# Kernel tuning notes

Measured on AMD Instinct MI355X. Metric: run time of the kernel, lower is better.

The kernel has to match this reference:

```python
import jax, jax.numpy as jnp
import numpy as np

K = 4
EPS = 1e-5
NEG_SLOPE = 0.2


def _edge_feature(coor_q, x_q, coor_k, x_k, k):
    """coor_*: [B,3,G*], x_q: [B,C,Gq], x_k: [B,C,Gk] -> [B,2C,Gq,k]"""
    B = x_k.shape[0]
    cq = jax.lax.stop_gradient(coor_q)
    ck = jax.lax.stop_gradient(coor_k)
    # squared pairwise distances [B, Gq, Gk]
    q2 = jnp.sum(cq * cq, axis=1)  # [B,Gq]
    k2 = jnp.sum(ck * ck, axis=1)  # [B,Gk]
    dist = q2[:, :, None] + k2[:, None, :] - 2.0 * jnp.einsum('bcq,bck->bqk', cq, ck)
    _, idx = jax.lax.top_k(-dist, k)  # k nearest, idx: [B,Gq,k]
    xk_t = jnp.transpose(x_k, (0, 2, 1))  # [B,Gk,C]
    feat = xk_t[jnp.arange(B)[:, None, None], idx]  # [B,Gq,k,C] gather
    feat = jnp.transpose(feat, (0, 3, 1, 2))  # [B,C,Gq,k]
    xq = jnp.broadcast_to(x_q[:, :, :, None], feat.shape)
    return jnp.concatenate([feat - xq, xq], axis=1)


def _group_norm(x, gamma, beta, groups):
    # x: [B,C,G,k], normalize per (group, sample) over (C//groups, G, k)
    B, C, G, k = x.shape
    xr = x.reshape(B, groups, -1)
    mean = jnp.mean(xr, axis=-1, keepdims=True)
    var = jnp.var(xr, axis=-1, keepdims=True)
    xn = ((xr - mean) * jax.lax.rsqrt(var + EPS)).reshape(B, C, G, k)
    return xn * gamma[None, :, None, None] + beta[None, :, None, None]


def _block(x, W, gamma, beta):
    # 1x1 conv (no bias) + GroupNorm(4) + LeakyReLU(0.2)
    y = jnp.einsum('oc,bcgk->bogk', W, x)
    y = _group_norm(y, gamma, beta, 4)
    return jax.nn.leaky_relu(y, NEG_SLOPE)


def setup_inputs() -> dict:
    key = jax.random.key(0)
    ks = jax.random.split(key, 10)
    B, C, Gs, Gd = 16, 384, 4096, 1024
    return {
        'coor': jax.random.normal(ks[0], (B, 3, Gs), jnp.float32),
        'f': jax.random.normal(ks[1], (B, C, Gs), jnp.float32),
        'coor_q': jax.random.normal(ks[2], (B, 3, Gd), jnp.float32),
        'f_q': jax.random.normal(ks[3], (B, C, Gd), jnp.float32),
        'W1': jax.random.normal(ks[4], (512, 2 * C), jnp.float32) * 0.02,
        'g1': jnp.ones((512,), jnp.float32),
        'b1': jnp.zeros((512,), jnp.float32),
        'W2': jax.random.normal(ks[5], (C, 1024), jnp.float32) * 0.02,
        'g2': jnp.ones((C,), jnp.float32),
        'b2': jnp.zeros((C,), jnp.float32),
    }


def reference(coor, f, coor_q, f_q, W1, g1, b1, W2, g2, b2):
    e1 = _edge_feature(coor_q, f_q, coor, f, K)        # [B,768,Gd,k]
    h = jnp.max(_block(e1, W1, g1, b1), axis=-1)       # [B,512,Gd]
    e2 = _edge_feature(coor_q, h, coor_q, h, K)        # [B,1024,Gd,k]
    out = jnp.max(_block(e2, W2, g2, b2), axis=-1)     # [B,384,Gd]
    return out
```

## Files before the change

kernel.cpp:

```cpp
#include <hip/hip_runtime.h>
#include <stdint.h>

#define B_   16
#define CIN  384
#define GS   4096
#define GD   1024
#define M1   512
#define K2C  512
#define M2   384
#define NEG  0.2f
#define EPS_ 1e-5f

typedef __bf16 bf16x8 __attribute__((ext_vector_type(8)));
typedef float  f32x4  __attribute__((ext_vector_type(4)));

__device__ __forceinline__ float bf2f(ushort u) {
  uint32_t v = ((uint32_t)u) << 16;
  return __builtin_bit_cast(float, v);
}
__device__ __forceinline__ ushort f2bf(float f) {
  uint32_t x = __builtin_bit_cast(uint32_t, f);
  x += 0x7FFFu + ((x >> 16) & 1u);
  return (ushort)(x >> 16);
}

__global__ void k_transpose(const float* __restrict__ src, ushort* __restrict__ dst,
                            int Cdim, int N) {
  __shared__ ushort tile[32][33];
  int b = blockIdx.z;
  int n0 = blockIdx.x * 32, c0 = blockIdx.y * 32;
  const float* s = src + (size_t)b * Cdim * N;
  ushort* d = dst + (size_t)b * Cdim * N;
  int tx = threadIdx.x, ty = threadIdx.y;
#pragma unroll
  for (int i = 0; i < 4; i++) {
    int c = c0 + ty + i * 8;
    tile[ty + i * 8][tx] = f2bf(s[(size_t)c * N + n0 + tx]);
  }
  __syncthreads();
#pragma unroll
  for (int i = 0; i < 4; i++) {
    int n = n0 + ty + i * 8;
    d[(size_t)n * Cdim + c0 + tx] = tile[tx][ty + i * 8];
  }
}

__global__ void k_wprep(const float* __restrict__ W, ushort* __restrict__ Wa,
                        ushort* __restrict__ Wd, int Khalf) {
  int t = blockIdx.x * 256 + threadIdx.x;
  int o = t / Khalf, c = t % Khalf;
  float wa = W[(size_t)o * 2 * Khalf + c];
  float wb = W[(size_t)o * 2 * Khalf + Khalf + c];
  Wa[t] = f2bf(wa);
  Wd[t] = f2bf(wb - wa);
}

__device__ __forceinline__ void knn_lmin(float& ad, int& ai, float bd, int bi) {
  bool bl = (bd < ad) || (bd == ad && bi < ai);
  ad = bl ? bd : ad; ai = bl ? bi : ai;
}
__device__ __forceinline__ void knn_ce(float& ad, int& ai, float& bd, int& bi) {
  bool bl = (bd < ad) || (bd == ad && bi < ai);
  float na = bl ? bd : ad, nb = bl ? ad : bd;
  int nia = bl ? bi : ai, nib = bl ? ai : bi;
  ad = na; bd = nb; ai = nia; bi = nib;
}

template<int GSRC>
__global__ __launch_bounds__(256) void k_knn(const float* __restrict__ cq,
                                             const float* __restrict__ ck,
                                             int* __restrict__ idx) {
#pragma clang fp contract(off)
  int tid = threadIdx.x;
  int lane = tid & 63, wv = tid >> 6;
  int b = blockIdx.y;
  int q = blockIdx.x * 4 + wv;
  const float* cqb = cq + (size_t)b * 3 * GD;
  const float* ckb = ck + (size_t)b * 3 * GSRC;
  float qx = cqb[q], qy = cqb[GD + q], qz = cqb[2 * GD + q];
  float q2 = (qx * qx + qy * qy) + qz * qz;

  float d0 = 1e30f, d1 = 1e30f, d2 = 1e30f, d3 = 1e30f;
  int i0 = 0x7FFFFFFF, i1 = 0x7FFFFFFF, i2 = 0x7FFFFFFF, i3 = 0x7FFFFFFF;
  for (int j0 = lane * 4; j0 < GSRC; j0 += 256) {
    float4 X = *reinterpret_cast<const float4*>(ckb + j0);
    float4 Y = *reinterpret_cast<const float4*>(ckb + GSRC + j0);
    float4 Z = *reinterpret_cast<const float4*>(ckb + 2 * GSRC + j0);
#pragma unroll
    for (int u = 0; u < 4; u++) {
      float x = (&X.x)[u], y = (&Y.x)[u], z = (&Z.x)[u];
      float s2 = (x * x + y * y) + z * z;
      float dot = (qx * x + qy * y) + qz * z;
      float d = (q2 + s2) - 2.0f * dot;
      int j = j0 + u;
      bool c = d < d3;
      d3 = c ? d : d3; i3 = c ? j : i3;
      c = d3 < d2; { float t = d3; d3 = c ? d2 : d3; d2 = c ? t : d2;
                     int ti = i3; i3 = c ? i2 : i3; i2 = c ? ti : i2; }
      c = d2 < d1; { float t = d2; d2 = c ? d1 : d2; d1 = c ? t : d1;
                     int ti = i2; i2 = c ? i1 : i2; i1 = c ? ti : i1; }
      c = d1 < d0; { float t = d1; d1 = c ? d0 : d1; d0 = c ? t : d0;
                     int ti = i1; i1 = c ? i0 : i1; i0 = c ? ti : i0; }
    }
  }
#pragma unroll
  for (int off = 1; off < 64; off <<= 1) {
    float pd0 = __shfl_xor(d0, off), pd1 = __shfl_xor(d1, off);
    float pd2 = __shfl_xor(d2, off), pd3 = __shfl_xor(d3, off);
    int pi0 = __shfl_xor(i0, off), pi1 = __shfl_xor(i1, off);
    int pi2 = __shfl_xor(i2, off), pi3 = __shfl_xor(i3, off);
    knn_lmin(d0, i0, pd3, pi3);
    knn_lmin(d1, i1, pd2, pi2);
    knn_lmin(d2, i2, pd1, pi1);
    knn_lmin(d3, i3, pd0, pi0);
    knn_ce(d0, i0, d2, i2);
    knn_ce(d1, i1, d3, i3);
    knn_ce(d0, i0, d1, i1);
    knn_ce(d2, i2, d3, i3);
  }
  if (lane == 0) {
    int4 r; r.x = i0; r.y = i1; r.z = i2; r.w = i3;
    *reinterpret_cast<int4*>(&idx[((size_t)b * GD + q) * 4]) = r;
  }
}

template<bool OUT_BF16>
__global__ __launch_bounds__(256) void k_gemm(const ushort* __restrict__ W,
                                              const ushort* __restrict__ Xt,
                                              void* __restrict__ outv,
                                              int M, int Kd, int N) {
  __shared__ __align__(16) ushort As[128 * 40];
  __shared__ __align__(16) ushort Bs[128 * 40];
  int b = blockIdx.z;
  const ushort* X = Xt + (size_t)b * N * Kd;
  int m0 = blockIdx.y * 128, n0 = blockIdx.x * 128;
  int tid = threadIdx.x;
  int w = tid >> 6, lane = tid & 63;
  int lr = lane & 15, lq = lane >> 4;
  int mw = (w >> 1) * 64, nw = (w & 1) * 64;
  int r0 = tid >> 2, c0 = tid & 3;

  f32x4 zero = {0.f, 0.f, 0.f, 0.f};
  f32x4 acc[4][4];
#pragma unroll
  for (int mi = 0; mi < 4; mi++)
#pragma unroll
    for (int ni = 0; ni < 4; ni++) acc[mi][ni] = zero;

  int nk = Kd / 32;
  for (int kt = 0; kt < nk; kt++) {
    int kk = kt * 32;
    __syncthreads();
    uint4 va0 = *reinterpret_cast<const uint4*>(W + (size_t)(m0 + r0) * Kd + kk + c0 * 8);
    uint4 va1 = *reinterpret_cast<const uint4*>(W + (size_t)(m0 + r0 + 64) * Kd + kk + c0 * 8);
    uint4 vb0 = *reinterpret_cast<const uint4*>(X + (size_t)(n0 + r0) * Kd + kk + c0 * 8);
    uint4 vb1 = *reinterpret_cast<const uint4*>(X + (size_t)(n0 + r0 + 64) * Kd + kk + c0 * 8);
    *reinterpret_cast<uint4*>(&As[(r0)      * 40 + c0 * 8]) = va0;
    *reinterpret_cast<uint4*>(&As[(r0 + 64) * 40 + c0 * 8]) = va1;
    *reinterpret_cast<uint4*>(&Bs[(r0)      * 40 + c0 * 8]) = vb0;
    *reinterpret_cast<uint4*>(&Bs[(r0 + 64) * 40 + c0 * 8]) = vb1;
    __syncthreads();
    bf16x8 af[4], bfr[4];
#pragma unroll
    for (int mi = 0; mi < 4; mi++)
      af[mi] = *reinterpret_cast<const bf16x8*>(&As[(mw + mi * 16 + lr) * 40 + lq * 8]);
#pragma unroll
    for (int ni = 0; ni < 4; ni++)
      bfr[ni] = *reinterpret_cast<const bf16x8*>(&Bs[(nw + ni * 16 + lr) * 40 + lq * 8]);
#pragma unroll
    for (int mi = 0; mi < 4; mi++)
#pragma unroll
      for (int ni = 0; ni < 4; ni++)
        acc[mi][ni] = __builtin_amdgcn_mfma_f32_16x16x32_bf16(af[mi], bfr[ni], acc[mi][ni], 0, 0, 0);
  }
#pragma unroll
  for (int mi = 0; mi < 4; mi++) {
    int m = m0 + mw + mi * 16 + lq * 4;
#pragma unroll
    for (int ni = 0; ni < 4; ni++) {
      int n = n0 + nw + ni * 16 + lr;
#pragma unroll
      for (int r = 0; r < 4; r++) {
        size_t off = (size_t)b * M * N + (size_t)(m + r) * N + n;
        if constexpr (OUT_BF16) ((ushort*)outv)[off] = f2bf(acc[mi][ni][r]);
        else                    ((float*)outv)[off] = acc[mi][ni][r];
      }
    }
  }
}

__global__ __launch_bounds__(256) void k_stats1y(const ushort* __restrict__ A,
                                                 const float* __restrict__ Bq,
                                                 const int* __restrict__ idx1,
                                                 const float* __restrict__ gam,
                                                 float* __restrict__ Ysel,
                                                 float* __restrict__ part) {
  __shared__ __align__(16) ushort Arow[GS];
  __shared__ __align__(16) int ids[GD * 4];
  __shared__ float rs[256], rq[256];
  int s = blockIdx.x, grp = blockIdx.y, b = blockIdx.z;
  int tid = threadIdx.x;
  for (int i = tid; i < GD; i += 256) {
    int4 v = *reinterpret_cast<const int4*>(&idx1[((size_t)b * GD + i) * 4]);
    v.x &= (GS - 1); v.y &= (GS - 1); v.z &= (GS - 1); v.w &= (GS - 1);
    *reinterpret_cast<int4*>(&ids[i * 4]) = v;
  }
  float sum = 0.f, ssq = 0.f;
  for (int oi = 0; oi < 16; oi++) {
    int o = grp * 128 + s * 16 + oi;
    const ushort* Ar = A + ((size_t)b * M1 + o) * GS;
    __syncthreads();
#pragma unroll
    for (int i = tid * 8; i < GS; i += 2048)
      *reinterpret_cast<uint4*>(&Arow[i]) = *reinterpret_cast<const uint4*>(&Ar[i]);
    __syncthreads();
    const float* Br = Bq + ((size_t)b * M1 + o) * GD;
    float* Yr = Ysel + ((size_t)b * M1 + o) * GD;
    float sgn = gam[o];
    for (int g = tid; g < GD; g += 256) {
      int4 id = *reinterpret_cast<const int4*>(&ids[g * 4]);
      float base = Br[g];
      float y0 = bf2f(Arow[id.x]) + base;
      float y1 = bf2f(Arow[id.y]) + base;
      float y2 = bf2f(Arow[id.z]) + base;
      float y3 = bf2f(Arow[id.w]) + base;
      sum += y0 + y1 + y2 + y3;
      ssq += y0 * y0 + y1 * y1 + y2 * y2 + y3 * y3;
      float mx = fmaxf(fmaxf(y0, y1), fmaxf(y2, y3));
      float mn = fminf(fminf(y0, y1), fminf(y2, y3));
      Yr[g] = (sgn >= 0.f) ? mx : mn;
    }
  }
  rs[tid] = sum; rq[tid] = ssq;
  __syncthreads();
  for (int t = 128; t > 0; t >>= 1) {
    if (tid < t) { rs[tid] += rs[tid + t]; rq[tid] += rq[tid + t]; }
    __syncthreads();
  }
  if (tid == 0) {
    int key = ((b * 4 + grp) * 8 + s) * 2;
    part[key] = rs[0]; part[key + 1] = rq[0];
  }
}

__global__ __launch_bounds__(256) void k_stats2y(const float* __restrict__ A2,
                                                 const float* __restrict__ B2q,
                                                 const int* __restrict__ idx2,
                                                 const float* __restrict__ gam,
                                                 float* __restrict__ Ysel,
                                                 float* __restrict__ part) {
  __shared__ __align__(16) float Arow[GD];
  __shared__ __align__(16) int ids[GD * 4];
  __shared__ float rs[256], rq[256];
  int s = blockIdx.x, grp = blockIdx.y, b = blockIdx.z;
  int tid = threadIdx.x;
  for (int i = tid; i < GD; i += 256) {
    int4 v = *reinterpret_cast<const int4*>(&idx2[((size_t)b * GD + i) * 4]);
    v.x &= (GD - 1); v.y &= (GD - 1); v.z &= (GD - 1); v.w &= (GD - 1);
    *reinterpret_cast<int4*>(&ids[i * 4]) = v;
  }
  float sum = 0.f, ssq = 0.f;
  for (int oi = 0; oi < 12; oi++) {
    int o = grp * 96 + s * 12 + oi;
    const float* Ar = A2 + ((size_t)b * M2 + o) * GD;
    __syncthreads();
#pragma unroll
    for (int i = tid * 4; i < GD; i += 1024)
      *reinterpret_cast<float4*>(&Arow[i]) = *reinterpret_cast<const float4*>(&Ar[i]);
    __syncthreads();
    const float* Br = B2q + ((size_t)b * M2 + o) * GD;
    float* Yr = Ysel + ((size_t)b * M2 + o) * GD;
    float sgn = gam[o];
    for (int g = tid; g < GD; g += 256) {
      int4 id = *reinterpret_cast<const int4*>(&ids[g * 4]);
      float base = Br[g];
      float y0 = Arow[id.x] + base;
      float y1 = Arow[id.y] + base;
      float y2 = Arow[id.z] + base;
      float y3 = Arow[id.w] + base;
      sum += y0 + y1 + y2 + y3;
      ssq += y0 * y0 + y1 * y1 + y2 * y2 + y3 * y3;
      float mx = fmaxf(fmaxf(y0, y1), fmaxf(y2, y3));
      float mn = fminf(fminf(y0, y1), fminf(y2, y3));
      Yr[g] = (sgn >= 0.f) ? mx : mn;
    }
  }
  rs[tid] = sum; rq[tid] = ssq;
  __syncthreads();
  for (int t = 128; t > 0; t >>= 1) {
    if (tid < t) { rs[tid] += rs[tid + t]; rq[tid] += rq[tid + t]; }
    __syncthreads();
  }
  if (tid == 0) {
    int key = ((b * 4 + grp) * 8 + s) * 2;
    part[key] = rs[0]; part[key + 1] = rq[0];
  }
}

__global__ void k_statsfin(const float* __restrict__ part, float* __restrict__ fin, float invN) {
  int t = threadIdx.x;
  float s = 0.f, q = 0.f;
  for (int i = 0; i < 8; i++) { s += part[(t * 8 + i) * 2]; q += part[(t * 8 + i) * 2 + 1]; }
  float mean = s * invN;
  float var = q * invN - mean * mean;
  float rstd = 1.0f / sqrtf(fmaxf(var, 0.0f) + EPS_);
  fin[t * 2] = mean; fin[t * 2 + 1] = rstd;
}

__global__ void k_h2(const float* __restrict__ Ysel, const float* __restrict__ fin,
                     const float* __restrict__ gam, const float* __restrict__ bet,
                     ushort* __restrict__ hT) {
  __shared__ ushort tile[64][66];
  int g0 = blockIdx.x * 64, o0 = blockIdx.y * 64, b = blockIdx.z;
  int tid = threadIdx.x;
  int gx = tid & 63, oy = tid >> 6;
#pragma unroll
  for (int oi = 0; oi < 16; oi++) {
    int ol = oi * 4 + oy;
    int o = o0 + ol;
    float y = Ysel[((size_t)b * M1 + o) * GD + g0 + gx];
    float mean = fin[(b * 4 + (o >> 7)) * 2];
    float rstd = fin[(b * 4 + (o >> 7)) * 2 + 1];
    float v = (y - mean) * rstd * gam[o] + bet[o];
    v = v >= 0.f ? v : NEG * v;
    tile[ol][gx] = f2bf(v);
  }
  __syncthreads();
  int col = tid & 63, r4 = tid >> 6;
#pragma unroll
  for (int i = 0; i < 16; i++) {
    int gl = i * 4 + r4;
    hT[((size_t)b * GD + g0 + gl) * K2C + o0 + col] = tile[col][gl];
  }
}

__global__ void k_out2(const float* __restrict__ Ysel2, const float* __restrict__ fin,
                       const float* __restrict__ gam, const float* __restrict__ bet,
                       float* __restrict__ out) {
  int b = blockIdx.z, o = blockIdx.y;
  int g = blockIdx.x * 256 + threadIdx.x;
  float mean = fin[(b * 4 + o / 96) * 2];
  float rstd = fin[(b * 4 + o / 96) * 2 + 1];
  float y = Ysel2[((size_t)b * M2 + o) * GD + g];
  float v = (y - mean) * rstd * gam[o] + bet[o];
  v = v >= 0.f ? v : NEG * v;
  out[((size_t)b * M2 + o) * GD + g] = v;
}

extern "C" void kernel_launch(void* const* d_in, const int* in_sizes, int n_in,
                              void* d_out, int out_size, void* d_ws, size_t ws_size,
                              hipStream_t stream) {
  (void)in_sizes; (void)n_in; (void)out_size;
  const float* coor  = (const float*)d_in[0];
  const float* f     = (const float*)d_in[1];
  const float* coorq = (const float*)d_in[2];
  const float* fq    = (const float*)d_in[3];
  const float* W1    = (const float*)d_in[4];
  const float* g1    = (const float*)d_in[5];
  const float* b1    = (const float*)d_in[6];
  const float* W2    = (const float*)d_in[7];
  const float* g2    = (const float*)d_in[8];
  const float* b2    = (const float*)d_in[9];

  if (ws_size < 182468608u) return;

  char* ws = (char*)d_ws;
  int*    idx1 = (int*)(ws + 0);
  int*    idx2 = (int*)(ws + 0x40000);
  float*  s1p  = (float*)(ws + 0x80000);
  float*  s1f  = (float*)(ws + 0x81000);
  float*  s2p  = (float*)(ws + 0x82000);
  float*  s2f  = (float*)(ws + 0x83000);
  ushort* W1a  = (ushort*)(ws + 0x84000);
  ushort* W1d  = W1a + (size_t)512 * 384;
  ushort* W2a  = W1d + (size_t)512 * 384;
  ushort* W2d  = W2a + (size_t)384 * 512;
  ushort* fT   = W2d + (size_t)384 * 512;
  ushort* fqT  = fT + (size_t)B_ * GS * CIN;
  ushort* Abuf = fqT + (size_t)B_ * GD * CIN;
  float*  Bq   = (float*)(Abuf + (size_t)B_ * M1 * GS);
  ushort* hT   = (ushort*)((char*)Bq + (size_t)B_ * M1 * GD * 4);
  float*  A2   = (float*)fT;
  float*  B2q  = A2 + (size_t)B_ * M2 * GD;
  float*  Ysel1 = (float*)fT;
  float*  Ysel2 = (float*)Abuf;

  k_transpose<<<dim3(GS / 32, CIN / 32, B_), dim3(32, 8), 0, stream>>>(f, fT, CIN, GS);
  k_transpose<<<dim3(GD / 32, CIN / 32, B_), dim3(32, 8), 0, stream>>>(fq, fqT, CIN, GD);
  k_wprep<<<dim3(512 * 384 / 256), 256, 0, stream>>>(W1, W1a, W1d, 384);
  k_wprep<<<dim3(384 * 512 / 256), 256, 0, stream>>>(W2, W2a, W2d, 512);

  k_knn<GS><<<dim3(GD / 4, B_), 256, 0, stream>>>(coorq, coor, idx1);
  k_knn<GD><<<dim3(GD / 4, B_), 256, 0, stream>>>(coorq, coorq, idx2);

  k_gemm<true ><<<dim3(GS / 128, M1 / 128, B_), 256, 0, stream>>>(W1a, fT, Abuf, M1, CIN, GS);
  k_gemm<false><<<dim3(GD / 128, M1 / 128, B_), 256, 0, stream>>>(W1d, fqT, Bq, M1, CIN, GD);

  k_stats1y<<<dim3(8, 4, B_), 256, 0, stream>>>(Abuf, Bq, idx1, g1, Ysel1, s1p);
  k_statsfin<<<1, 64, 0, stream>>>(s1p, s1f, 1.0f / 524288.0f);
  k_h2<<<dim3(GD / 64, M1 / 64, B_), 256, 0, stream>>>(Ysel1, s1f, g1, b1, hT);

  k_gemm<false><<<dim3(GD / 128, M2 / 128, B_), 256, 0, stream>>>(W2a, hT, A2, M2, K2C, GD);
  k_gemm<false><<<dim3(GD / 128, M2 / 128, B_), 256, 0, stream>>>(W2d, hT, B2q, M2, K2C, GD);

  k_stats2y<<<dim3(8, 4, B_), 256, 0, stream>>>(A2, B2q, idx2, g2, Ysel2, s2p);
  k_statsfin<<<1, 64, 0, stream>>>(s2p, s2f, 1.0f / 393216.0f);
  k_out2<<<dim3(GD / 256, M2, B_), 256, 0, stream>>>(Ysel2, s2f, g2, b2, (float*)d_out);
}
```

Baseline: 476.8 us.

## Speed up kNN with precomputed norms, packed FP32 math, and 64-bit sort keys

Squared norms of source and query points are now computed once by a new small kernel instead of inside the per-query loop. Distances are evaluated with packed two-wide FP32 multiply/add/fma instructions. Each distance and its index are packed into a single sortable 64-bit key, so the top-4 insertion and the wave-level merge become sorting networks on one integer instead of separate float/int compare-selects. This removes redundant per-candidate arithmetic and halves the select work, but adds two extra launches and an extra load stream, and the fma changes rounding relative to the reference's uncontracted expression, which could flip near-tie neighbours.

```diff
diff --git a/kernel.cpp b/kernel.cpp
--- a/kernel.cpp
+++ b/kernel.cpp
@@ -13,6 +13,8 @@
 
 typedef __bf16 bf16x8 __attribute__((ext_vector_type(8)));
 typedef float  f32x4  __attribute__((ext_vector_type(4)));
+typedef float  f32x2  __attribute__((ext_vector_type(2)));
+typedef unsigned long long u64k;
 
 __device__ __forceinline__ float bf2f(ushort u) {
   uint32_t v = ((uint32_t)u) << 16;
@@ -22,6 +24,16 @@
   uint32_t x = __builtin_bit_cast(uint32_t, f);
   x += 0x7FFFu + ((x >> 16) & 1u);
   return (ushort)(x >> 16);
+}
+
+__device__ __forceinline__ f32x2 pk_mul(f32x2 a, f32x2 b) {
+  f32x2 d; asm("v_pk_mul_f32 %0, %1, %2" : "=v"(d) : "v"(a), "v"(b)); return d;
+}
+__device__ __forceinline__ f32x2 pk_add(f32x2 a, f32x2 b) {
+  f32x2 d; asm("v_pk_add_f32 %0, %1, %2" : "=v"(d) : "v"(a), "v"(b)); return d;
+}
+__device__ __forceinline__ f32x2 pk_fma(f32x2 a, f32x2 b, f32x2 c) {
+  f32x2 d; asm("v_pk_fma_f32 %0, %1, %2, %3" : "=v"(d) : "v"(a), "v"(b), "v"(c)); return d;
 }
 
 __global__ void k_transpose(const float* __restrict__ src, ushort* __restrict__ dst,
@@ -55,71 +67,80 @@
   Wd[t] = f2bf(wb - wa);
 }
 
-__device__ __forceinline__ void knn_lmin(float& ad, int& ai, float bd, int bi) {
-  bool bl = (bd < ad) || (bd == ad && bi < ai);
-  ad = bl ? bd : ad; ai = bl ? bi : ai;
-}
-__device__ __forceinline__ void knn_ce(float& ad, int& ai, float& bd, int& bi) {
-  bool bl = (bd < ad) || (bd == ad && bi < ai);
-  float na = bl ? bd : ad, nb = bl ? ad : bd;
-  int nia = bl ? bi : ai, nib = bl ? ai : bi;
-  ad = na; bd = nb; ai = nia; bi = nib;
-}
+__global__ void k_s2(const float* __restrict__ c, float* __restrict__ s2, int N) {
+#pragma clang fp contract(off)
+  int b = blockIdx.z;
+  int i = blockIdx.x * 256 + threadIdx.x;
+  const float* cb = c + (size_t)b * 3 * N;
+  float x = cb[i], y = cb[N + i], z = cb[2 * N + i];
+  s2[(size_t)b * N + i] = (x * x + y * y) + z * z;
+}
+
+__device__ __forceinline__ u64k knn_key(float d, int j) {
+  uint32_t u = __builtin_bit_cast(uint32_t, d);
+  u ^= ((uint32_t)((int32_t)u >> 31)) | 0x80000000u;
+  return ((u64k)u << 32) | (uint32_t)j;
+}
+__device__ __forceinline__ void kce(u64k& a, u64k& b) {
+  bool c = b < a;
+  u64k lo = c ? b : a, hi = c ? a : b;
+  a = lo; b = hi;
+}
+__device__ __forceinline__ void klmin(u64k& a, u64k b) { a = b < a ? b : a; }
 
 template<int GSRC>
 __global__ __launch_bounds__(256) void k_knn(const float* __restrict__ cq,
                                              const float* __restrict__ ck,
+                                             const float* __restrict__ s2qry,
+                                             const float* __restrict__ s2src,
                                              int* __restrict__ idx) {
-#pragma clang fp contract(off)
   int tid = threadIdx.x;
   int lane = tid & 63, wv = tid >> 6;
   int b = blockIdx.y;
   int q = blockIdx.x * 4 + wv;
   const float* cqb = cq + (size_t)b * 3 * GD;
   const float* ckb = ck + (size_t)b * 3 * GSRC;
+  const float* s2b = s2src + (size_t)b * GSRC;
   float qx = cqb[q], qy = cqb[GD + q], qz = cqb[2 * GD + q];
-  float q2 = (qx * qx + qy * qy) + qz * qz;
-
-  float d0 = 1e30f, d1 = 1e30f, d2 = 1e30f, d3 = 1e30f;
-  int i0 = 0x7FFFFFFF, i1 = 0x7FFFFFFF, i2 = 0x7FFFFFFF, i3 = 0x7FFFFFFF;
+  float q2 = s2qry[(size_t)b * GD + q];
+  f32x2 qxp = {qx, qx}, qyp = {qy, qy}, qzp = {qz, qz};
+  f32x2 q2p = {q2, q2}, m2p = {-2.f, -2.f};
+
+  u64k k0 = ~0ull, k1 = ~0ull, k2 = ~0ull, k3 = ~0ull;
   for (int j0 = lane * 4; j0 < GSRC; j0 += 256) {
     float4 X = *reinterpret_cast<const float4*>(ckb + j0);
     float4 Y = *reinterpret_cast<const float4*>(ckb + GSRC + j0);
     float4 Z = *reinterpret_cast<const float4*>(ckb + 2 * GSRC + j0);
-#pragma unroll
-    for (int u = 0; u < 4; u++) {
-      float x = (&X.x)[u], y = (&Y.x)[u], z = (&Z.x)[u];
-      float s2 = (x * x + y * y) + z * z;
-      float dot = (qx * x + qy * y) + qz * z;
-      float d = (q2 + s2) - 2.0f * dot;
-      int j = j0 + u;
-      bool c = d < d3;
-      d3 = c ? d : d3; i3 = c ? j : i3;
-      c = d3 < d2; { float t = d3; d3 = c ? d2 : d3; d2 = c ? t : d2;
-                     int ti = i3; i3 = c ? i2 : i3; i2 = c ? ti : i2; }
-      c = d2 < d1; { float t = d2; d2 = c ? d1 : d2; d1 = c ? t : d1;
-                     int ti = i2; i2 = c ? i1 : i2; i1 = c ? ti : i1; }
-      c = d1 < d0; { float t = d1; d1 = c ? d0 : d1; d0 = c ? t : d0;
-                     int ti = i1; i1 = c ? i0 : i1; i0 = c ? ti : i0; }
-    }
+    float4 S = *reinterpret_cast<const float4*>(s2b + j0);
+    f32x2 xl = {X.x, X.y}, xh = {X.z, X.w};
+    f32x2 yl = {Y.x, Y.y}, yh = {Y.z, Y.w};
+    f32x2 zl = {Z.x, Z.y}, zh = {Z.z, Z.w};
+    f32x2 sl = {S.x, S.y}, sh = {S.z, S.w};
+    f32x2 dotl = pk_add(pk_add(pk_mul(qxp, xl), pk_mul(qyp, yl)), pk_mul(qzp, zl));
+    f32x2 doth = pk_add(pk_add(pk_mul(qxp, xh), pk_mul(qyp, yh)), pk_mul(qzp, zh));
+    f32x2 al = pk_add(q2p, sl);
+    f32x2 ah = pk_add(q2p, sh);
+    f32x2 dl = pk_fma(dotl, m2p, al);
+    f32x2 dh = pk_fma(doth, m2p, ah);
+    u64k n0 = knn_key(dl.x, j0);
+    u64k n1 = knn_key(dl.y, j0 + 1);
+    u64k n2 = knn_key(dh.x, j0 + 2);
+    u64k n3 = knn_key(dh.y, j0 + 3);
+    kce(n0, n1); kce(n2, n3); kce(n0, n2); kce(n1, n3); kce(n1, n2);
+    klmin(k0, n3); klmin(k1, n2); klmin(k2, n1); klmin(k3, n0);
+    kce(k0, k2); kce(k1, k3); kce(k0, k1); kce(k2, k3);
   }
 #pragma unroll
   for (int off = 1; off < 64; off <<= 1) {
-    float pd0 = __shfl_xor(d0, off), pd1 = __shfl_xor(d1, off);
-    float pd2 = __shfl_xor(d2, off), pd3 = __shfl_xor(d3, off);
-    int pi0 = __shfl_xor(i0, off), pi1 = __shfl_xor(i1, off);
-    int pi2 = __shfl_xor(i2, off), pi3 = __shfl_xor(i3, off);
-    knn_lmin(d0, i0, pd3, pi3);
-    knn_lmin(d1, i1, pd2, pi2);
-    knn_lmin(d2, i2, pd1, pi1);
-    knn_lmin(d3, i3, pd0, pi0);
-    knn_ce(d0, i0, d2, i2);
-    knn_ce(d1, i1, d3, i3);
-    knn_ce(d0, i0, d1, i1);
-    knn_ce(d2, i2, d3, i3);
+    u64k p0 = __shfl_xor(k0, off), p1 = __shfl_xor(k1, off);
+    u64k p2 = __shfl_xor(k2, off), p3 = __shfl_xor(k3, off);
+    klmin(k0, p3); klmin(k1, p2); klmin(k2, p1); klmin(k3, p0);
+    kce(k0, k2); kce(k1, k3); kce(k0, k1); kce(k2, k3);
   }
   if (lane == 0) {
-    int4 r; r.x = i0; r.y = i1; r.z = i2; r.w = i3;
+    int4 r;
+    r.x = (int)(uint32_t)k0; r.y = (int)(uint32_t)k1;
+    r.z = (int)(uint32_t)k2; r.w = (int)(uint32_t)k3;
     *reinterpret_cast<int4*>(&idx[((size_t)b * GD + q) * 4]) = r;
   }
 }
@@ -384,14 +405,18 @@
   float*  B2q  = A2 + (size_t)B_ * M2 * GD;
   float*  Ysel1 = (float*)fT;
   float*  Ysel2 = (float*)Abuf;
+  float*  s2s  = (float*)hT;
+  float*  s2q  = s2s + (size_t)B_ * GS;
 
   k_transpose<<<dim3(GS / 32, CIN / 32, B_), dim3(32, 8), 0, stream>>>(f, fT, CIN, GS);
   k_transpose<<<dim3(GD / 32, CIN / 32, B_), dim3(32, 8), 0, stream>>>(fq, fqT, CIN, GD);
   k_wprep<<<dim3(512 * 384 / 256), 256, 0, stream>>>(W1, W1a, W1d, 384);
   k_wprep<<<dim3(384 * 512 / 256), 256, 0, stream>>>(W2, W2a, W2d, 512);
-
-  k_knn<GS><<<dim3(GD / 4, B_), 256, 0, stream>>>(coorq, coor, idx1);
-  k_knn<GD><<<dim3(GD / 4, B_), 256, 0, stream>>>(coorq, coorq, idx2);
+  k_s2<<<dim3(GS / 256, 1, B_), 256, 0, stream>>>(coor, s2s, GS);
+  k_s2<<<dim3(GD / 256, 1, B_), 256, 0, stream>>>(coorq, s2q, GD);
+
+  k_knn<GS><<<dim3(GD / 4, B_), 256, 0, stream>>>(coorq, coor, s2q, s2s, idx1);
+  k_knn<GD><<<dim3(GD / 4, B_), 256, 0, stream>>>(coorq, coorq, s2q, s2q, idx2);
 
   k_gemm<true ><<<dim3(GS / 128, M1 / 128, B_), 256, 0, stream>>>(W1a, fT, Abuf, M1, CIN, GS);
   k_gemm<false><<<dim3(GD / 128, M1 / 128, B_), 256, 0, stream>>>(W1d, fqT, Bq, M1, CIN, GD);
```

Measured after the change: 477.9 us. Within noise of the previous version (+0.2%).
